# Optimization experiments

Measured on AMD Instinct MI355X. Metric: run time of the kernel, lower is better.

The kernel has to match this reference:

```python
import jax, jax.numpy as jnp
import numpy as np

IN_FEATURES = 4096
OUT_FEATURES = 4096
SHARED_ROWS = 512
BATCH = 4096


def setup_inputs() -> dict:
    key = jax.random.key(0)
    k1, k2, k3 = jax.random.split(key, 3)
    x = jax.random.normal(k1, (BATCH, IN_FEATURES), dtype=jnp.float32)
    shared_weights = jax.random.normal(k2, (SHARED_ROWS, IN_FEATURES), dtype=jnp.float32)
    bias = jax.random.normal(k3, (OUT_FEATURES,), dtype=jnp.float32)
    return {"x": x, "shared_weights": shared_weights, "bias": bias}


def reference(x, shared_weights, bias):
    # Original: W = shared_weights.repeat(out_features // shared_rows, 1)  -> [out, in]
    #           y = x @ W.T + bias
    # Row i of W equals shared_weights[i % shared_rows], so the output columns are a
    # tile of the small GEMM result — compute the small GEMM once and tile (same math,
    # avoids materializing the full [out, in] weight).
    reps = OUT_FEATURES // SHARED_ROWS
    y_small = jnp.einsum("bi,ri->br", x, shared_weights)  # [batch, shared_rows]
    y = jnp.tile(y_small, (1, reps)) + bias  # [batch, out_features]
    return y
```

## Files before the change

### kernel.cpp

```cpp
#include <hip/hip_runtime.h>
#include <hip/hip_bf16.h>


typedef __bf16 bf8 __attribute__((ext_vector_type(8)));
typedef float f16v __attribute__((ext_vector_type(16)));
typedef unsigned int uint;
typedef unsigned short ushort;

constexpr int M = 4096;
constexpr int K = 4096;
constexpr int NS = 512;
constexpr int OUTF = 4096;
constexpr int BM = 64, BN = 64, BK = 64;
constexpr int NITER = K / BK;
constexpr int SSTR = 68;
constexpr int WSTR = 16 * SSTR;

#define PERM_HI2(hi, lo) __builtin_amdgcn_perm((hi), (lo), 0x07060302u)
#define WAITCNT_VM4 0xF74
#define WAITCNT_VM0 0xF70

__device__ __forceinline__ void async16(const ushort* g, ushort* l) {
  __builtin_amdgcn_global_load_lds(
      (const __attribute__((address_space(1))) void*)g,
      (__attribute__((address_space(3))) void*)l, 16, 0, 0);
}

__global__ __launch_bounds__(256)
void convert_kernel(const float* __restrict__ x, const float* __restrict__ w,
                    ushort* __restrict__ xb, ushort* __restrict__ wb) {
  const size_t i = (size_t)blockIdx.x * 256 + threadIdx.x;
  constexpr size_t NX = (size_t)M * K / 8;
  const float* src;
  ushort* dst;
  if (i < NX) { src = x + i * 8; dst = xb + i * 8; }
  else        { const size_t j = i - NX; src = w + j * 8; dst = wb + j * 8; }
  const uint4 a = *reinterpret_cast<const uint4*>(src);
  const uint4 b = *reinterpret_cast<const uint4*>(src + 4);
  uint4 o;
  o.x = PERM_HI2(a.y, a.x); o.y = PERM_HI2(a.w, a.z);
  o.z = PERM_HI2(b.y, b.x); o.w = PERM_HI2(b.w, b.z);
  *reinterpret_cast<uint4*>(dst) = o;
}

__global__ __launch_bounds__(256, 2)
void gemm_kernel(const ushort* __restrict__ xb, const ushort* __restrict__ wb,
                 const float* __restrict__ bias, float* __restrict__ out) {
  __shared__ __align__(16) ushort As[3][BM * BK];
  __shared__ __align__(16) ushort Bs[3][BN * BK];

  const int b  = blockIdx.x;
  const int mt = ((b >> 6) << 3) | (b & 7);
  const int nt = (b >> 3) & 7;

  const int tid  = threadIdx.x;
  const int wv   = tid >> 6;
  const int lane = tid & 63;

  int goff[2], lloc[2];
#pragma unroll
  for (int j = 0; j < 2; ++j) {
    const int c = (wv * 2 + j) * 64 + lane;
    const int r = c >> 3;
    const int g = (c & 7) ^ (r & 7);
    goff[j] = r * K + g * 8;
    lloc[j] = (wv * 2 + j) * 512;
  }

  const ushort* xT = xb + (size_t)(mt * BM) * K;
  const ushort* wT = wb + (size_t)(nt * BN) * K;

  auto issue = [&](int tile, int stage) {
    const int ko = tile * BK;
#pragma unroll
    for (int j = 0; j < 2; ++j) {
      async16(xT + ko + goff[j], &As[stage][lloc[j]]);
      async16(wT + ko + goff[j], &Bs[stage][lloc[j]]);
    }
  };

  const int l31 = lane & 31;
  const int hi  = lane >> 5;
  const int coff = ((2 * wv + hi) ^ (lane & 7)) * 8;

  f16v acc[2][2] = {};

  issue(0, 0);
  issue(1, 1);

  int st = 0;
  for (int kk = 0; kk < NITER; ++kk) {
    if (kk + 1 < NITER) __builtin_amdgcn_s_waitcnt(WAITCNT_VM4);
    else                __builtin_amdgcn_s_waitcnt(WAITCNT_VM0);
    __builtin_amdgcn_s_barrier();
    asm volatile("" ::: "memory");

    if (kk + 2 < NITER) {
      int st2 = st + 2; if (st2 >= 3) st2 -= 3;
      issue(kk + 2, st2);
    }

    const ushort* aT = As[st];
    const ushort* bT = Bs[st];
    const bf8 a0 = *reinterpret_cast<const bf8*>(&aT[(l31)      * BK + coff]);
    const bf8 a1 = *reinterpret_cast<const bf8*>(&aT[(32 + l31) * BK + coff]);
    const bf8 b0 = *reinterpret_cast<const bf8*>(&bT[(l31)      * BK + coff]);
    const bf8 b1 = *reinterpret_cast<const bf8*>(&bT[(32 + l31) * BK + coff]);
    acc[0][0] = __builtin_amdgcn_mfma_f32_32x32x16_bf16(a0, b0, acc[0][0], 0, 0, 0);
    acc[0][1] = __builtin_amdgcn_mfma_f32_32x32x16_bf16(a0, b1, acc[0][1], 0, 0, 0);
    acc[1][0] = __builtin_amdgcn_mfma_f32_32x32x16_bf16(a1, b0, acc[1][0], 0, 0, 0);
    acc[1][1] = __builtin_amdgcn_mfma_f32_32x32x16_bf16(a1, b1, acc[1][1], 0, 0, 0);
    asm volatile("" ::: "memory");

    if (++st >= 3) st = 0;
  }

  __syncthreads();
  float* scr = reinterpret_cast<float*>(&As[0][0]);

  const int c4  = tid & 15;
  const int r16 = tid >> 4;
  const float4* bias4 = reinterpret_cast<const float4*>(bias);
  float4 bb[8];
#pragma unroll
  for (int rep = 0; rep < 8; ++rep)
    bb[rep] = bias4[rep * 128 + nt * 16 + c4];

#pragma unroll
  for (int rq = 0; rq < 4; ++rq) {
    const int tm = rq >> 1, half = rq & 1;
#pragma unroll
    for (int tn = 0; tn < 2; ++tn)
#pragma unroll
      for (int j = 0; j < 8; ++j) {
        const int row16 = (j & 3) + 8 * (j >> 2) + 4 * hi;
        scr[wv * WSTR + row16 * SSTR + tn * 32 + l31] = acc[tm][tn][8 * half + j];
      }
    __syncthreads();
    float4 s;
    {
      const float4 p0 = *reinterpret_cast<const float4*>(&scr[0 * WSTR + r16 * SSTR + c4 * 4]);
      const float4 p1 = *reinterpret_cast<const float4*>(&scr[1 * WSTR + r16 * SSTR + c4 * 4]);
      const float4 p2 = *reinterpret_cast<const float4*>(&scr[2 * WSTR + r16 * SSTR + c4 * 4]);
      const float4 p3 = *reinterpret_cast<const float4*>(&scr[3 * WSTR + r16 * SSTR + c4 * 4]);
      s.x = (p0.x + p1.x) + (p2.x + p3.x);
      s.y = (p0.y + p1.y) + (p2.y + p3.y);
      s.z = (p0.z + p1.z) + (p2.z + p3.z);
      s.w = (p0.w + p1.w) + (p2.w + p3.w);
    }
    float* orow = out + (size_t)(mt * BM + rq * 16 + r16) * OUTF + nt * BN + c4 * 4;
#pragma unroll
    for (int rep = 0; rep < 8; ++rep) {
      float4 o;
      o.x = s.x + bb[rep].x; o.y = s.y + bb[rep].y;
      o.z = s.z + bb[rep].z; o.w = s.w + bb[rep].w;
      *reinterpret_cast<float4*>(orow + rep * NS) = o;
    }
    __syncthreads();
  }
}

extern "C" void kernel_launch(void* const* d_in, const int* in_sizes, int n_in,
                              void* d_out, int out_size, void* d_ws, size_t ws_size,
                              hipStream_t stream) {
  (void)in_sizes; (void)n_in; (void)out_size; (void)ws_size;
  const float* x    = (const float*)d_in[0];
  const float* w    = (const float*)d_in[1];
  const float* bias = (const float*)d_in[2];
  float* out = (float*)d_out;

  ushort* xb = (ushort*)d_ws;
  ushort* wb = (ushort*)d_ws + (size_t)M * K;

  constexpr int conv_blocks = (int)(((size_t)M * K / 8 + (size_t)NS * K / 8) / 256);
  convert_kernel<<<dim3(conv_blocks), dim3(256), 0, stream>>>(x, w, xb, wb);
  gemm_kernel<<<dim3(64 * 8), dim3(256), 0, stream>>>(xb, wb, bias, out);
}
```

Measured before the change: 161.6 us.

## Fuse x fp32-to-bf16 conversion into GEMM loads with register-staged double buffering

The GEMM now reads x as fp32 directly, converts it to bf16 in registers and writes it to LDS, so the separate pass that converted all of x to bf16 is dropped. Only the small shared weight is still pre-converted. The async global-to-LDS triple-buffered pipeline is replaced by a register-prefetch, LDS double-buffered scheme. This removes a full read/write pass over x, but the GEMM now fetches twice as many bytes for x and stages them through VGPRs, which may expose more load latency.

```diff
diff --git a/kernel.cpp b/kernel.cpp
--- a/kernel.cpp
+++ b/kernel.cpp
@@ -17,24 +17,12 @@
 constexpr int WSTR = 16 * SSTR;
 
 #define PERM_HI2(hi, lo) __builtin_amdgcn_perm((hi), (lo), 0x07060302u)
-#define WAITCNT_VM4 0xF74
-#define WAITCNT_VM0 0xF70
-
-__device__ __forceinline__ void async16(const ushort* g, ushort* l) {
-  __builtin_amdgcn_global_load_lds(
-      (const __attribute__((address_space(1))) void*)g,
-      (__attribute__((address_space(3))) void*)l, 16, 0, 0);
-}
 
 __global__ __launch_bounds__(256)
-void convert_kernel(const float* __restrict__ x, const float* __restrict__ w,
-                    ushort* __restrict__ xb, ushort* __restrict__ wb) {
+void convert_w(const float* __restrict__ w, ushort* __restrict__ wb) {
   const size_t i = (size_t)blockIdx.x * 256 + threadIdx.x;
-  constexpr size_t NX = (size_t)M * K / 8;
-  const float* src;
-  ushort* dst;
-  if (i < NX) { src = x + i * 8; dst = xb + i * 8; }
-  else        { const size_t j = i - NX; src = w + j * 8; dst = wb + j * 8; }
+  const float* src = w + i * 8;
+  ushort* dst = wb + i * 8;
   const uint4 a = *reinterpret_cast<const uint4*>(src);
   const uint4 b = *reinterpret_cast<const uint4*>(src + 4);
   uint4 o;
@@ -44,10 +32,11 @@
 }
 
 __global__ __launch_bounds__(256, 2)
-void gemm_kernel(const ushort* __restrict__ xb, const ushort* __restrict__ wb,
+void gemm_kernel(const float* __restrict__ x, const ushort* __restrict__ wb,
                  const float* __restrict__ bias, float* __restrict__ out) {
-  __shared__ __align__(16) ushort As[3][BM * BK];
-  __shared__ __align__(16) ushort Bs[3][BN * BK];
+  __shared__ __align__(16) ushort sh[2 * BM * BK + 2 * BN * BK];
+  ushort* As = sh;
+  ushort* Bs = sh + 2 * BM * BK;
 
   const int b  = blockIdx.x;
   const int mt = ((b >> 6) << 3) | (b & 7);
@@ -56,27 +45,50 @@
   const int tid  = threadIdx.x;
   const int wv   = tid >> 6;
   const int lane = tid & 63;
+  const int lr   = lane & 15;
+  const int lq   = lane >> 4;
+  const int gB   = lane & 7;
 
-  int goff[2], lloc[2];
+  int rA[4], ldsA[4];
+#pragma unroll
+  for (int j = 0; j < 4; ++j) {
+    rA[j] = wv * 16 + j * 4 + lq;
+    ldsA[j] = (rA[j] * 8 + ((lr >> 1) ^ (rA[j] & 7))) * 8 + (lr & 1) * 4;
+  }
+  int rB[2], ldsB[2];
 #pragma unroll
   for (int j = 0; j < 2; ++j) {
-    const int c = (wv * 2 + j) * 64 + lane;
-    const int r = c >> 3;
-    const int g = (c & 7) ^ (r & 7);
-    goff[j] = r * K + g * 8;
-    lloc[j] = (wv * 2 + j) * 512;
+    rB[j] = (wv * 2 + j) * 8 + (lane >> 3);
+    ldsB[j] = (rB[j] * 8 + (gB ^ (rB[j] & 7))) * 8;
   }
 
-  const ushort* xT = xb + (size_t)(mt * BM) * K;
+  const float*  xT = x  + (size_t)(mt * BM) * K;
   const ushort* wT = wb + (size_t)(nt * BN) * K;
 
-  auto issue = [&](int tile, int stage) {
+  uint4 ar[4], br[2];
+
+  auto loadT = [&](int tile) {
     const int ko = tile * BK;
 #pragma unroll
-    for (int j = 0; j < 2; ++j) {
-      async16(xT + ko + goff[j], &As[stage][lloc[j]]);
-      async16(wT + ko + goff[j], &Bs[stage][lloc[j]]);
+    for (int j = 0; j < 4; ++j)
+      ar[j] = *reinterpret_cast<const uint4*>(xT + (size_t)rA[j] * K + ko + lr * 4);
+#pragma unroll
+    for (int j = 0; j < 2; ++j)
+      br[j] = *reinterpret_cast<const uint4*>(wT + (size_t)rB[j] * K + ko + gB * 8);
+  };
+  auto writeT = [&](int stg) {
+    ushort* Ad = As + stg * (BM * BK);
+    ushort* Bd = Bs + stg * (BN * BK);
+#pragma unroll
+    for (int j = 0; j < 4; ++j) {
+      uint2 o;
+      o.x = PERM_HI2(ar[j].y, ar[j].x);
+      o.y = PERM_HI2(ar[j].w, ar[j].z);
+      *reinterpret_cast<uint2*>(Ad + ldsA[j]) = o;
     }
+#pragma unroll
+    for (int j = 0; j < 2; ++j)
+      *reinterpret_cast<uint4*>(Bd + ldsB[j]) = br[j];
   };
 
   const int l31 = lane & 31;
@@ -85,23 +97,18 @@
 
   f16v acc[2][2] = {};
 
-  issue(0, 0);
-  issue(1, 1);
+  loadT(0);
+  writeT(0);
+  loadT(1);
+  asm volatile("s_waitcnt lgkmcnt(0)" ::: "memory");
 
   int st = 0;
   for (int kk = 0; kk < NITER; ++kk) {
-    if (kk + 1 < NITER) __builtin_amdgcn_s_waitcnt(WAITCNT_VM4);
-    else                __builtin_amdgcn_s_waitcnt(WAITCNT_VM0);
     __builtin_amdgcn_s_barrier();
     asm volatile("" ::: "memory");
 
-    if (kk + 2 < NITER) {
-      int st2 = st + 2; if (st2 >= 3) st2 -= 3;
-      issue(kk + 2, st2);
-    }
-
-    const ushort* aT = As[st];
-    const ushort* bT = Bs[st];
+    const ushort* aT = As + st * (BM * BK);
+    const ushort* bT = Bs + st * (BN * BK);
     const bf8 a0 = *reinterpret_cast<const bf8*>(&aT[(l31)      * BK + coff]);
     const bf8 a1 = *reinterpret_cast<const bf8*>(&aT[(32 + l31) * BK + coff]);
     const bf8 b0 = *reinterpret_cast<const bf8*>(&bT[(l31)      * BK + coff]);
@@ -112,11 +119,16 @@
     acc[1][1] = __builtin_amdgcn_mfma_f32_32x32x16_bf16(a1, b1, acc[1][1], 0, 0, 0);
     asm volatile("" ::: "memory");
 
-    if (++st >= 3) st = 0;
+    if (kk + 1 < NITER) {
+      writeT(st ^ 1);
+      if (kk + 2 < NITER) loadT(kk + 2);
+      asm volatile("s_waitcnt lgkmcnt(0)" ::: "memory");
+    }
+    st ^= 1;
   }
 
   __syncthreads();
-  float* scr = reinterpret_cast<float*>(&As[0][0]);
+  float* scr = reinterpret_cast<float*>(sh);
 
   const int c4  = tid & 15;
   const int r16 = tid >> 4;
@@ -169,10 +181,9 @@
   const float* bias = (const float*)d_in[2];
   float* out = (float*)d_out;
 
-  ushort* xb = (ushort*)d_ws;
-  ushort* wb = (ushort*)d_ws + (size_t)M * K;
+  ushort* wb = (ushort*)d_ws;
 
-  constexpr int conv_blocks = (int)(((size_t)M * K / 8 + (size_t)NS * K / 8) / 256);
-  convert_kernel<<<dim3(conv_blocks), dim3(256), 0, stream>>>(x, w, xb, wb);
-  gemm_kernel<<<dim3(64 * 8), dim3(256), 0, stream>>>(xb, wb, bias, out);
+  constexpr int convw_blocks = (int)((size_t)NS * K / 8 / 256);
+  convert_w<<<dim3(convw_blocks), dim3(256), 0, stream>>>(w, wb);
+  gemm_kernel<<<dim3(64 * 8), dim3(256), 0, stream>>>(x, wb, bias, out);
 }
```

Result: slower. 230.0 us (+42.3%).
